# Optimization experiments

Measured on AMD Instinct MI355X. Metric: run time of the kernel, lower is better.

## Reference

```python
import jax, jax.numpy as jnp
import numpy as np

B, S, E, H = 4, 8192, 512, 8
D = E // H  # head_dim = 64


def setup_inputs() -> dict:
    key = jax.random.key(0)
    ks = jax.random.split(key, 9)
    scale = 1.0 / np.sqrt(E)
    x = jax.random.normal(ks[0], (B, S, E), dtype=jnp.float32)
    # torch nn.Linear convention: y = x @ W.T + b, W has shape (out, in)
    Wp = jax.random.uniform(ks[1], (E, E), jnp.float32, -scale, scale)
    bp = jax.random.uniform(ks[2], (E,), jnp.float32, -scale, scale)
    Wc = jax.random.uniform(ks[3], (E, E), jnp.float32, -scale, scale)
    bc = jax.random.uniform(ks[4], (E,), jnp.float32, -scale, scale)
    Ws = jax.random.uniform(ks[5], (E, E), jnp.float32, -scale, scale)
    bs = jax.random.uniform(ks[6], (E,), jnp.float32, -scale, scale)
    Wo = jax.random.uniform(ks[7], (E, E), jnp.float32, -scale, scale)
    bo = jax.random.uniform(ks[8], (E,), jnp.float32, -scale, scale)
    return {"x": x, "Wp": Wp, "bp": bp, "Wc": Wc, "bc": bc,
            "Ws": Ws, "bs": bs, "Wo": Wo, "bo": bo}


def reference(x, Wp, bp, Wc, bc, Ws, bs, Wo, bo):
    # Faithful to TreeAttention.forward with tree_structure=None (default path).
    # NOTE: original views projections as (B,S,H,D) without transposing head/seq,
    # so the matmuls mix HEADS per token (HxH scores), not tokens.
    b, s, _ = x.shape
    parent = (jnp.einsum('bse,fe->bsf', x, Wp) + bp).reshape(b, s, H, D)
    child = (jnp.einsum('bse,fe->bsf', x, Wc) + bc).reshape(b, s, H, D)
    sibling = (jnp.einsum('bse,fe->bsf', x, Ws) + bs).reshape(b, s, H, D)
    # per-token head-mixing scores: (B, S, H, H)
    scores = jnp.einsum('bshd,bstd->bsht', parent, child) / jnp.sqrt(
        jnp.asarray(D, dtype=x.dtype))
    attention = jax.nn.softmax(scores, axis=-1)
    # dropout is identity in eval mode (reference runs in inference mode)
    out = jnp.einsum('bsht,bstd->bshd', attention, sibling).reshape(b, s, E)
    return jnp.einsum('bse,fe->bsf', out, Wo) + bo
```

## Files before the change

kernel.cpp:

```cpp
#include <hip/hip_runtime.h>
#include <hip/hip_bf16.h>

typedef unsigned short u16;
typedef __attribute__((ext_vector_type(8))) short bf16x8;
typedef __attribute__((ext_vector_type(4))) float f32x4;
typedef __attribute__((ext_vector_type(8))) unsigned short u16x8;

#define GLDS(gp, lp) __builtin_amdgcn_global_load_lds( \
    (const __attribute__((address_space(1))) void*)(gp), \
    (__attribute__((address_space(3))) void*)(lp), 16, 0, 0)

__device__ __forceinline__ u16 f2b(float f) {
  unsigned u = __builtin_bit_cast(unsigned, f);
  return (u16)((u + 0x7fffu + ((u >> 16) & 1u)) >> 16);
}
__device__ __forceinline__ float b2f(u16 s) {
  return __builtin_bit_cast(float, (unsigned)s << 16);
}

#define BARX() do { __builtin_amdgcn_sched_barrier(0); \
  asm volatile("s_barrier" ::: "memory"); \
  __builtin_amdgcn_sched_barrier(0); } while (0)

__global__ __launch_bounds__(256) void convert_k(
    const float* __restrict__ x, const float* __restrict__ Wp,
    const float* __restrict__ Wc, const float* __restrict__ Ws,
    const float* __restrict__ Wo, u16* __restrict__ xb,
    u16* __restrict__ wall, u16* __restrict__ wob)
{
  const long CX = 2097152;
  const long CW = 98304;
  const long CO = 32768;
  const long total = CX + CW + CO;
  for (long i = (long)blockIdx.x * blockDim.x + threadIdx.x; i < total;
       i += (long)gridDim.x * blockDim.x) {
    const float* src; u16* dst;
    if (i < CX) {
      src = x + i * 8; dst = xb + i * 8;
    } else if (i < CX + CW) {
      long e = (i - CX) * 8;
      int n = (int)(e >> 9), k = (int)(e & 511);
      const float* wr = (n < 512)  ? (Wp + (long)n * 512)
                      : (n < 1024) ? (Wc + (long)(n - 512) * 512)
                                   : (Ws + (long)(n - 1024) * 512);
      src = wr + k;
      dst = wall + (long)(n >> 4) * 8192 + (k >> 3) * 128 + (n & 15) * 8;
    } else {
      long e = (i - CX - CW) * 8;
      int n = (int)(e >> 9), k = (int)(e & 511);
      src = Wo + e;
      dst = wob + (long)(n >> 4) * 8192 + (k >> 3) * 128 + (n & 15) * 8;
    }
    f32x4 v0 = *(const f32x4*)src;
    f32x4 v1 = *(const f32x4*)(src + 4);
    u16x8 o;
    o[0]=f2b(v0[0]); o[1]=f2b(v0[1]); o[2]=f2b(v0[2]); o[3]=f2b(v0[3]);
    o[4]=f2b(v1[0]); o[5]=f2b(v1[1]); o[6]=f2b(v1[2]); o[7]=f2b(v1[3]);
    *(u16x8*)dst = o;
  }
}

template<int NC, bool BF16OUT>
__global__ __launch_bounds__(512, 2) void gemm8(
    const u16* __restrict__ A, const u16* __restrict__ Bw,
    const float* __restrict__ bias0, const float* __restrict__ bias1,
    const float* __restrict__ bias2, void* __restrict__ Cout)
{
  __shared__ alignas(16) char smem[65536];
  char* sAc = smem;

  const int tid = threadIdx.x;
  const int w = tid >> 6, lane = tid & 63;
  const int wr = w >> 2, wc = w & 3;
  const int ln15 = lane & 15, g4 = lane >> 4, l7 = lane & 7;

  const int nbx = NC / 256;
  const int nwg = nbx * 128;
  const int qq = nwg / 8;
  const int flat = blockIdx.x;
  const int swz = (flat & 7) * qq + (flat >> 3);
  const int bx = swz % nbx, by = swz / nbx;
  const long row0 = (long)by * 256;
  const int col0 = bx * 256;

  const int t8 = tid >> 3;
  const int gsw = (tid & 7) ^ (t8 & 7);
  const u16* pA = A + (row0 + t8) * 512 + gsw * 8;

#define STG_A(h, t) do { \
    const u16* s_ = pA + (h) * 32768 + (t) * 64; \
    char* d_ = sAc + (h) * 16384 + w * 1024; \
    GLDS(s_, d_); GLDS(s_ + 65536, d_ + 8192); \
  } while (0)

  const int gkb0 = (g4 ^ l7) << 4;
  const int gkb1 = ((g4 + 4) ^ l7) << 4;
  const int aoff = (wr * 64 + ln15) * 128;

#define LOAD_A(MH) do { \
    const char* ba_ = sAc + (MH) * 16384 + aoff; \
    _Pragma("unroll") for (int mf = 0; mf < 4; ++mf) { \
      aF[mf][0] = *(const bf16x8*)(ba_ + mf * 2048 + gkb0); \
      aF[mf][1] = *(const bf16x8*)(ba_ + mf * 2048 + gkb1); \
    } } while (0)

  const u16* pBg = Bw + ((long)(col0 >> 4) + wc * 4) * 8192 + g4 * 128 + ln15 * 8;

#define GLB_B(NH, BF, t) do { \
    _Pragma("unroll") for (int nf = 0; nf < 2; ++nf) \
    _Pragma("unroll") for (int kk = 0; kk < 2; ++kk) \
      BF[nf][kk] = *(const bf16x8*)(pBg + ((NH) * 2 + nf) * 8192 + ((t) * 8 + kk * 4) * 128); \
  } while (0)

#define MFMA_Q(MH, NH, BF) do { \
    __builtin_amdgcn_s_setprio(1); \
    _Pragma("unroll") for (int mf = 0; mf < 4; ++mf) \
    _Pragma("unroll") for (int nf = 0; nf < 2; ++nf) { \
      f32x4 c_ = acc[(MH) * 4 + mf][(NH) * 2 + nf]; \
      c_ = __builtin_amdgcn_mfma_f32_16x16x32_bf16(aF[mf][0], BF[nf][0], c_, 0, 0, 0); \
      c_ = __builtin_amdgcn_mfma_f32_16x16x32_bf16(aF[mf][1], BF[nf][1], c_, 0, 0, 0); \
      acc[(MH) * 4 + mf][(NH) * 2 + nf] = c_; \
    } \
    __builtin_amdgcn_s_setprio(0); \
  } while (0)
#define VMW(nstr) asm volatile("s_waitcnt vmcnt(" nstr ")" ::: "memory")

  f32x4 acc[8][4] = {};

  STG_A(0, 0); STG_A(1, 0);

  for (int t = 0; t < 8; ++t) {
    const bool st = (t < 7);
    bf16x8 aF[4][2], bFa[2][2], bFb[2][2];

    VMW("2"); BARX();
    GLB_B(0, bFa, t); GLB_B(1, bFb, t);
    LOAD_A(0);
    MFMA_Q(0, 0, bFa);
    BARX();
    if (st) STG_A(0, t + 1);
    MFMA_Q(0, 1, bFb);
    VMW("2"); BARX();
    LOAD_A(1);
    MFMA_Q(1, 1, bFb);
    BARX();
    if (st) STG_A(1, t + 1);
    MFMA_Q(1, 0, bFa);
  }

  __syncthreads();
  const long rgb = row0 + wr * 128;
  const int cgb = col0 + wc * 64;
  if (BF16OUT) {
    u16* sc = (u16*)(smem + (w << 13));
#pragma unroll
    for (int h2 = 0; h2 < 2; ++h2) {
#pragma unroll
      for (int n = 0; n < 4; ++n) {
        const int colg = cgb + ln15 + n * 16;
        const float* bp_ = (NC == 512) ? bias0
                           : (colg < 512 ? bias0 : (colg < 1024 ? bias1 : bias2));
        const float bv = bp_[colg & 511];
        const int c = ln15 + n * 16;
        const int gsl = c >> 3, co = c & 7;
#pragma unroll
        for (int mf = 0; mf < 4; ++mf)
#pragma unroll
          for (int j = 0; j < 4; ++j) {
            const int r = mf * 16 + (g4 << 2) + j;
            sc[r * 64 + (((gsl ^ (r & 7)) << 3) | co)] = f2b(acc[h2 * 4 + mf][n][j] + bv);
          }
      }
      asm volatile("s_waitcnt lgkmcnt(0)" ::: "memory");
      __builtin_amdgcn_sched_barrier(0);
#pragma unroll
      for (int it = 0; it < 8; ++it) {
        const int rr = it * 8 + (lane >> 3);
        const int gl = lane & 7;
        u16x8 v = *(const u16x8*)(sc + rr * 64 + ((gl ^ (rr & 7)) << 3));
        *(u16x8*)((u16*)Cout + (rgb + h2 * 64 + rr) * NC + cgb + gl * 8) = v;
      }
      asm volatile("s_waitcnt lgkmcnt(0)" ::: "memory");
      __builtin_amdgcn_sched_barrier(0);
    }
  } else {
    float* scf = (float*)(smem + (w << 13));
#pragma unroll
    for (int q = 0; q < 4; ++q) {
#pragma unroll
      for (int n = 0; n < 4; ++n) {
        const int colg = cgb + ln15 + n * 16;
        const float bv = bias0[colg & 511];
        const int c = ln15 + n * 16;
        const int gsl = c >> 2, co = c & 3;
#pragma unroll
        for (int mh = 0; mh < 2; ++mh)
#pragma unroll
          for (int j = 0; j < 4; ++j) {
            const int r = mh * 16 + (g4 << 2) + j;
            scf[r * 64 + (((gsl ^ (r & 7)) << 2) | co)] = acc[q * 2 + mh][n][j] + bv;
          }
      }
      asm volatile("s_waitcnt lgkmcnt(0)" ::: "memory");
      __builtin_amdgcn_sched_barrier(0);
#pragma unroll
      for (int it = 0; it < 8; ++it) {
        const int rr = it * 4 + (lane >> 4);
        const int gl = lane & 15;
        f32x4 v = *(const f32x4*)(scf + rr * 64 + ((gl ^ (rr & 7)) << 2));
        *(f32x4*)((float*)Cout + (rgb + q * 32 + rr) * NC + cgb + gl * 4) = v;
      }
      asm volatile("s_waitcnt lgkmcnt(0)" ::: "memory");
      __builtin_amdgcn_sched_barrier(0);
    }
  }
#undef STG_A
#undef LOAD_A
#undef GLB_B
#undef MFMA_Q
#undef VMW
}

__global__ __launch_bounds__(256) void attn_k(const u16* __restrict__ PCS,
                                              u16* __restrict__ OUT)
{
  __shared__ float L[4][1664];
  const int w = threadIdx.x >> 6, lane = threadIdx.x & 63;
  const long token = (long)blockIdx.x * 4 + w;
  float* Lw = L[w];
  const int C0 = 544, S0 = 1088, AT0 = 1600;
  const u16* rowp = PCS + token * 1536;
#pragma unroll
  for (int q = 0; q < 3; ++q) {
    u16x8 v = *(const u16x8*)(rowp + q * 512 + lane * 8);
    float* dst = (q < 2) ? (Lw + q * 544 + (lane >> 3) * 68 + (lane & 7) * 8)
                         : (Lw + S0 + lane * 8);
    f32x4 a = {b2f(v[0]), b2f(v[1]), b2f(v[2]), b2f(v[3])};
    f32x4 b = {b2f(v[4]), b2f(v[5]), b2f(v[6]), b2f(v[7])};
    *(f32x4*)dst = a;
    *(f32x4*)(dst + 4) = b;
  }
  const int h = lane >> 3, t = lane & 7;
  float sc = 0.f;
#pragma unroll
  for (int d = 0; d < 64; d += 4) {
    f32x4 pv = *(const f32x4*)(Lw + h * 68 + d);
    f32x4 cv = *(const f32x4*)(Lw + C0 + t * 68 + d);
    sc += pv[0]*cv[0] + pv[1]*cv[1] + pv[2]*cv[2] + pv[3]*cv[3];
  }
  sc *= 0.125f;
  float mx = sc;
  mx = fmaxf(mx, __shfl_xor(mx, 1));
  mx = fmaxf(mx, __shfl_xor(mx, 2));
  mx = fmaxf(mx, __shfl_xor(mx, 4));
  float e = __expf(sc - mx);
  float sm = e;
  sm += __shfl_xor(sm, 1);
  sm += __shfl_xor(sm, 2);
  sm += __shfl_xor(sm, 4);
  Lw[AT0 + lane] = e / sm;
  float o[8] = {0, 0, 0, 0, 0, 0, 0, 0};
#pragma unroll
  for (int tt = 0; tt < 8; ++tt) {
    const float av = Lw[AT0 + h * 8 + tt];
    f32x4 s0 = *(const f32x4*)(Lw + S0 + tt * 64 + t * 8);
    f32x4 s1 = *(const f32x4*)(Lw + S0 + tt * 64 + t * 8 + 4);
    o[0] += av * s0[0]; o[1] += av * s0[1]; o[2] += av * s0[2]; o[3] += av * s0[3];
    o[4] += av * s1[0]; o[5] += av * s1[1]; o[6] += av * s1[2]; o[7] += av * s1[3];
  }
  u16x8 ov;
#pragma unroll
  for (int j = 0; j < 8; ++j) ov[j] = f2b(o[j]);
  *(u16x8*)(OUT + token * 512 + lane * 8) = ov;
}

extern "C" void kernel_launch(void* const* d_in, const int* in_sizes, int n_in,
                              void* d_out, int out_size, void* d_ws, size_t ws_size,
                              hipStream_t stream) {
  const float* x  = (const float*)d_in[0];
  const float* Wp = (const float*)d_in[1];
  const float* bp = (const float*)d_in[2];
  const float* Wc = (const float*)d_in[3];
  const float* bc = (const float*)d_in[4];
  const float* Ws = (const float*)d_in[5];
  const float* bs = (const float*)d_in[6];
  const float* Wo = (const float*)d_in[7];
  const float* bo = (const float*)d_in[8];

  char* ws = (char*)d_ws;
  u16* xb   = (u16*)ws;
  u16* wall = (u16*)(ws + 33554432);
  u16* wob  = (u16*)(ws + 35127296);
  u16* pcs  = (u16*)(ws + 35651584);
  u16* outb = xb;

  convert_k<<<2048, 256, 0, stream>>>(x, Wp, Wc, Ws, Wo, xb, wall, wob);
  gemm8<1536, true><<<768, 512, 0, stream>>>(xb, wall, bp, bc, bs, pcs);
  attn_k<<<8192, 256, 0, stream>>>(pcs, outb);
  gemm8<512, false><<<256, 512, 0, stream>>>(outb, wob, bo, bo, bo, d_out);
}
```

Before: 135.1 us.

## Replace 256x256 GEMM with 128x128 tile staging both operands through LDS

The GEMM kernel moves from 256x256 tiles with 8 waves (B fragments loaded directly from a pre-tiled global layout) to 128x128 tiles with 4 waves. Both A and B are now staged through LDS with global_load_lds, and the weight conversion writes plain row-major bf16 instead of the tiled layout. This shrinks LDS to 32KB and raises the block count and occupancy per CU. In exchange it loses the intra-iteration split pipelining and reuses each staged tile over fewer outputs. The single-buffered loop now waits on vmcnt(0) every k-step.

```diff
diff --git a/kernel.cpp b/kernel.cpp
--- a/kernel.cpp
+++ b/kernel.cpp
@@ -43,13 +43,9 @@
       const float* wr = (n < 512)  ? (Wp + (long)n * 512)
                       : (n < 1024) ? (Wc + (long)(n - 512) * 512)
                                    : (Ws + (long)(n - 1024) * 512);
-      src = wr + k;
-      dst = wall + (long)(n >> 4) * 8192 + (k >> 3) * 128 + (n & 15) * 8;
+      src = wr + k; dst = wall + e;
     } else {
-      long e = (i - CX - CW) * 8;
-      int n = (int)(e >> 9), k = (int)(e & 511);
-      src = Wo + e;
-      dst = wob + (long)(n >> 4) * 8192 + (k >> 3) * 128 + (n & 15) * 8;
+      long e = (i - CX - CW) * 8; src = Wo + e; dst = wob + e;
     }
     f32x4 v0 = *(const f32x4*)src;
     f32x4 v1 = *(const f32x4*)(src + 4);
@@ -61,132 +57,116 @@
 }
 
 template<int NC, bool BF16OUT>
-__global__ __launch_bounds__(512, 2) void gemm8(
+__global__ __launch_bounds__(256, 3) void gemmT(
     const u16* __restrict__ A, const u16* __restrict__ Bw,
     const float* __restrict__ bias0, const float* __restrict__ bias1,
     const float* __restrict__ bias2, void* __restrict__ Cout)
 {
-  __shared__ alignas(16) char smem[65536];
+  __shared__ alignas(16) char smem[32768];
   char* sAc = smem;
+  char* sBc = smem + 16384;
 
   const int tid = threadIdx.x;
   const int w = tid >> 6, lane = tid & 63;
-  const int wr = w >> 2, wc = w & 3;
+  const int wr = w >> 1, wc = w & 1;
   const int ln15 = lane & 15, g4 = lane >> 4, l7 = lane & 7;
 
-  const int nbx = NC / 256;
-  const int nwg = nbx * 128;
+  const int nbx = NC / 128;
+  const int nwg = nbx * 256;
   const int qq = nwg / 8;
   const int flat = blockIdx.x;
   const int swz = (flat & 7) * qq + (flat >> 3);
   const int bx = swz % nbx, by = swz / nbx;
-  const long row0 = (long)by * 256;
-  const int col0 = bx * 256;
+  const long row0 = (long)by * 128;
+  const int col0 = bx * 128;
 
   const int t8 = tid >> 3;
   const int gsw = (tid & 7) ^ (t8 & 7);
   const u16* pA = A + (row0 + t8) * 512 + gsw * 8;
-
-#define STG_A(h, t) do { \
-    const u16* s_ = pA + (h) * 32768 + (t) * 64; \
-    char* d_ = sAc + (h) * 16384 + w * 1024; \
-    GLDS(s_, d_); GLDS(s_ + 65536, d_ + 8192); \
+  const u16* pB = Bw + ((long)col0 + t8) * 512 + gsw * 8;
+
+#define STG(tt) do { \
+    const u16* a_ = pA + (tt) * 64; const u16* b_ = pB + (tt) * 64; \
+    char* da_ = sAc + w * 1024; char* db_ = sBc + w * 1024; \
+    GLDS(a_, da_);                GLDS(a_ + 16384, da_ + 4096); \
+    GLDS(a_ + 32768, da_ + 8192); GLDS(a_ + 49152, da_ + 12288); \
+    GLDS(b_, db_);                GLDS(b_ + 16384, db_ + 4096); \
+    GLDS(b_ + 32768, db_ + 8192); GLDS(b_ + 49152, db_ + 12288); \
   } while (0)
 
   const int gkb0 = (g4 ^ l7) << 4;
   const int gkb1 = ((g4 + 4) ^ l7) << 4;
-  const int aoff = (wr * 64 + ln15) * 128;
-
-#define LOAD_A(MH) do { \
-    const char* ba_ = sAc + (MH) * 16384 + aoff; \
-    _Pragma("unroll") for (int mf = 0; mf < 4; ++mf) { \
-      aF[mf][0] = *(const bf16x8*)(ba_ + mf * 2048 + gkb0); \
-      aF[mf][1] = *(const bf16x8*)(ba_ + mf * 2048 + gkb1); \
-    } } while (0)
-
-  const u16* pBg = Bw + ((long)(col0 >> 4) + wc * 4) * 8192 + g4 * 128 + ln15 * 8;
-
-#define GLB_B(NH, BF, t) do { \
-    _Pragma("unroll") for (int nf = 0; nf < 2; ++nf) \
-    _Pragma("unroll") for (int kk = 0; kk < 2; ++kk) \
-      BF[nf][kk] = *(const bf16x8*)(pBg + ((NH) * 2 + nf) * 8192 + ((t) * 8 + kk * 4) * 128); \
-  } while (0)
-
-#define MFMA_Q(MH, NH, BF) do { \
-    __builtin_amdgcn_s_setprio(1); \
-    _Pragma("unroll") for (int mf = 0; mf < 4; ++mf) \
-    _Pragma("unroll") for (int nf = 0; nf < 2; ++nf) { \
-      f32x4 c_ = acc[(MH) * 4 + mf][(NH) * 2 + nf]; \
-      c_ = __builtin_amdgcn_mfma_f32_16x16x32_bf16(aF[mf][0], BF[nf][0], c_, 0, 0, 0); \
-      c_ = __builtin_amdgcn_mfma_f32_16x16x32_bf16(aF[mf][1], BF[nf][1], c_, 0, 0, 0); \
-      acc[(MH) * 4 + mf][(NH) * 2 + nf] = c_; \
-    } \
-    __builtin_amdgcn_s_setprio(0); \
-  } while (0)
-#define VMW(nstr) asm volatile("s_waitcnt vmcnt(" nstr ")" ::: "memory")
-
-  f32x4 acc[8][4] = {};
-
-  STG_A(0, 0); STG_A(1, 0);
-
+  const char* fA = sAc + (wr * 64 + ln15) * 128;
+  const char* fB = sBc + (wc * 64 + ln15) * 128;
+
+  f32x4 acc[4][4] = {};
+
+  STG(0);
   for (int t = 0; t < 8; ++t) {
-    const bool st = (t < 7);
-    bf16x8 aF[4][2], bFa[2][2], bFb[2][2];
-
-    VMW("2"); BARX();
-    GLB_B(0, bFa, t); GLB_B(1, bFb, t);
-    LOAD_A(0);
-    MFMA_Q(0, 0, bFa);
+    bf16x8 aF[4][2], bF[4][2];
+    asm volatile("s_waitcnt vmcnt(0)" ::: "memory");
     BARX();
-    if (st) STG_A(0, t + 1);
-    MFMA_Q(0, 1, bFb);
-    VMW("2"); BARX();
-    LOAD_A(1);
-    MFMA_Q(1, 1, bFb);
+#pragma unroll
+    for (int mf = 0; mf < 4; ++mf) {
+      aF[mf][0] = *(const bf16x8*)(fA + mf * 2048 + gkb0);
+      aF[mf][1] = *(const bf16x8*)(fA + mf * 2048 + gkb1);
+    }
+#pragma unroll
+    for (int nf = 0; nf < 4; ++nf) {
+      bF[nf][0] = *(const bf16x8*)(fB + nf * 2048 + gkb0);
+      bF[nf][1] = *(const bf16x8*)(fB + nf * 2048 + gkb1);
+    }
+    asm volatile("s_waitcnt lgkmcnt(0)" ::: "memory");
     BARX();
-    if (st) STG_A(1, t + 1);
-    MFMA_Q(1, 0, bFa);
+    if (t < 7) STG(t + 1);
+    __builtin_amdgcn_sched_barrier(0);
+    __builtin_amdgcn_s_setprio(1);
+#pragma unroll
+    for (int mf = 0; mf < 4; ++mf)
+#pragma unroll
+      for (int nf = 0; nf < 4; ++nf) {
+        f32x4 c_ = acc[mf][nf];
+        c_ = __builtin_amdgcn_mfma_f32_16x16x32_bf16(aF[mf][0], bF[nf][0], c_, 0, 0, 0);
+        c_ = __builtin_amdgcn_mfma_f32_16x16x32_bf16(aF[mf][1], bF[nf][1], c_, 0, 0, 0);
+        acc[mf][nf] = c_;
+      }
+    __builtin_amdgcn_s_setprio(0);
   }
 
   __syncthreads();
-  const long rgb = row0 + wr * 128;
+  const long rgb = row0 + wr * 64;
   const int cgb = col0 + wc * 64;
   if (BF16OUT) {
     u16* sc = (u16*)(smem + (w << 13));
 #pragma unroll
-    for (int h2 = 0; h2 < 2; ++h2) {
-#pragma unroll
-      for (int n = 0; n < 4; ++n) {
-        const int colg = cgb + ln15 + n * 16;
-        const float* bp_ = (NC == 512) ? bias0
-                           : (colg < 512 ? bias0 : (colg < 1024 ? bias1 : bias2));
-        const float bv = bp_[colg & 511];
-        const int c = ln15 + n * 16;
-        const int gsl = c >> 3, co = c & 7;
-#pragma unroll
-        for (int mf = 0; mf < 4; ++mf)
-#pragma unroll
-          for (int j = 0; j < 4; ++j) {
-            const int r = mf * 16 + (g4 << 2) + j;
-            sc[r * 64 + (((gsl ^ (r & 7)) << 3) | co)] = f2b(acc[h2 * 4 + mf][n][j] + bv);
-          }
-      }
-      asm volatile("s_waitcnt lgkmcnt(0)" ::: "memory");
-      __builtin_amdgcn_sched_barrier(0);
-#pragma unroll
-      for (int it = 0; it < 8; ++it) {
-        const int rr = it * 8 + (lane >> 3);
-        const int gl = lane & 7;
-        u16x8 v = *(const u16x8*)(sc + rr * 64 + ((gl ^ (rr & 7)) << 3));
-        *(u16x8*)((u16*)Cout + (rgb + h2 * 64 + rr) * NC + cgb + gl * 8) = v;
-      }
-      asm volatile("s_waitcnt lgkmcnt(0)" ::: "memory");
-      __builtin_amdgcn_sched_barrier(0);
+    for (int n = 0; n < 4; ++n) {
+      const int colg = cgb + ln15 + n * 16;
+      const float* bp_ = (NC == 512) ? bias0
+                         : (colg < 512 ? bias0 : (colg < 1024 ? bias1 : bias2));
+      const float bv = bp_[colg & 511];
+      const int c = ln15 + n * 16;
+      const int gsl = c >> 3, co = c & 7;
+#pragma unroll
+      for (int mf = 0; mf < 4; ++mf)
+#pragma unroll
+        for (int j = 0; j < 4; ++j) {
+          const int r = mf * 16 + (g4 << 2) + j;
+          sc[r * 64 + (((gsl ^ (r & 7)) << 3) | co)] = f2b(acc[mf][n][j] + bv);
+        }
+    }
+    asm volatile("s_waitcnt lgkmcnt(0)" ::: "memory");
+    __builtin_amdgcn_sched_barrier(0);
+#pragma unroll
+    for (int it = 0; it < 8; ++it) {
+      const int rr = it * 8 + (lane >> 3);
+      const int gl = lane & 7;
+      u16x8 v = *(const u16x8*)(sc + rr * 64 + ((gl ^ (rr & 7)) << 3));
+      *(u16x8*)((u16*)Cout + (rgb + rr) * NC + cgb + gl * 8) = v;
     }
   } else {
     float* scf = (float*)(smem + (w << 13));
 #pragma unroll
-    for (int q = 0; q < 4; ++q) {
+    for (int q = 0; q < 2; ++q) {
 #pragma unroll
       for (int n = 0; n < 4; ++n) {
         const int colg = cgb + ln15 + n * 16;
@@ -214,11 +194,7 @@
       __builtin_amdgcn_sched_barrier(0);
     }
   }
-#undef STG_A
-#undef LOAD_A
-#undef GLB_B
-#undef MFMA_Q
-#undef VMW
+#undef STG
 }
 
 __global__ __launch_bounds__(256) void attn_k(const u16* __restrict__ PCS,
@@ -295,7 +271,7 @@
   u16* outb = xb;
 
   convert_k<<<2048, 256, 0, stream>>>(x, Wp, Wc, Ws, Wo, xb, wall, wob);
-  gemm8<1536, true><<<768, 512, 0, stream>>>(xb, wall, bp, bc, bs, pcs);
+  gemmT<1536, true><<<3072, 256, 0, stream>>>(xb, wall, bp, bc, bs, pcs);
   attn_k<<<8192, 256, 0, stream>>>(pcs, outb);
-  gemm8<512, false><<<256, 512, 0, stream>>>(outb, wob, bo, bo, bo, d_out);
-}
+  gemmT<512, false><<<1024, 256, 0, stream>>>(outb, wob, bo, bo, bo, d_out);
+}
```

Measured after the change: 139.4 us. 1.03x slower.
